# Kernel optimization log

Hardware: AMD Instinct MI355X
Metric: run time of the kernel (lower is better)

## Reference

```python
import jax, jax.numpy as jnp
import numpy as np

WEIGHT_SCALE = 0.02  # matches torch.randn(...)*0.02 init

def setup_inputs() -> dict:
    key = jax.random.key(0)
    k1, k2, k3, k4 = jax.random.split(key, 4)
    B, D = 16384, 1024
    x_re = jax.random.normal(k1, (B, D), dtype=jnp.float32)
    x_im = jax.random.normal(k2, (B, D), dtype=jnp.float32)
    w_re = jax.random.normal(k3, (D, D), dtype=jnp.float32) * WEIGHT_SCALE
    w_im = jax.random.normal(k4, (D, D), dtype=jnp.float32) * WEIGHT_SCALE
    return {"x_re": x_re, "x_im": x_im, "w_re": w_re, "w_im": w_im}

def reference(x_re, x_im, w_re, w_im):
    x = jax.lax.complex(x_re, x_im)            # [B, D] complex64
    W = jax.lax.complex(w_re, w_im)            # [D, D] complex64
    # Skew-Hermitian part: A = W - W^H
    A = W - jnp.conj(W.T)
    D = W.shape[0]
    I = jnp.eye(D, dtype=W.dtype)
    # Cayley transform: U = (I - A)^{-1} (I + A)  (unitary)
    U = jnp.linalg.solve(I - A, I + A)
    # Original: x @ U.transpose(-1, -2) (plain transpose, no conj)
    return x @ U.T
```

## Files before the change

### kernel.cpp

```cpp
#include <hip/hip_runtime.h>
#include <hip/hip_bf16.h>

#define DD 1024
#define NB 16384
#define SZ (DD * DD)
#define CHB 512

typedef unsigned short u16;
typedef __attribute__((ext_vector_type(4))) float f32x4;
typedef __attribute__((ext_vector_type(8))) short short8;
typedef __attribute__((ext_vector_type(4))) short short4v;

__device__ __forceinline__ u16 f32_bf16(float f) {
  unsigned u = __builtin_bit_cast(unsigned, f);
  u += 0x7FFFu + ((u >> 16) & 1u);
  return (u16)(u >> 16);
}
__device__ __forceinline__ float bf16_f32(u16 h) {
  unsigned u = ((unsigned)h) << 16;
  return __builtin_bit_cast(float, u);
}
__device__ __forceinline__ void gload16(const void* g, void* l) {
  __builtin_amdgcn_global_load_lds(
      (const __attribute__((address_space(1))) unsigned int*)g,
      (__attribute__((address_space(3))) unsigned int*)l, 16, 0, 0);
}

struct CArgs {
  const u16 *Ar[3], *Ai[3];
  const u16 *Br[3], *Bi[3];
  int nseg;
  float alpha, g1, g2, ddiag;
  const u16 *e1r, *e1i, *e2r, *e2i;
  u16 *hi_n_re, *hi_n_im, *lo_n_re, *lo_n_im;
  u16 *t1_re, *t1_im;
  u16 *t2_re, *t2_im;
  u16 *lt_re, *lt_im;
  int t_ldt;
  unsigned t1_xi;
  const float *cxr, *cxi; u16 *cxb;
  int cm0a, cm1a, cm0b, cm1b;
};

__global__ __launch_bounds__(256) void zchain(CArgs g) {
  constexpr int SA = 64 * 32, SB = 32 * 32;
  constexpr int SLOT = 2 * SA + 2 * SB;
  __shared__ __align__(16) u16 smem[4 * SLOT];
  const int tid = threadIdx.x;

  if ((int)blockIdx.x >= CHB) {
    int nra = g.cm1a - g.cm0a;
    int tot = nra + (g.cm1b - g.cm0b);
    for (int r = (int)blockIdx.x - CHB; r < tot; r += 256) {
      int m = (r < nra) ? (g.cm0a + r) : (g.cm0b + r - nra);
      f32x4 v = ((const f32x4*)g.cxr)[m * 256 + tid];
      short4v s;
      #pragma unroll
      for (int e = 0; e < 4; ++e) s[e] = (short)f32_bf16(v[e]);
      ((short4v*)g.cxb)[m * 512 + tid] = s;
      f32x4 w = ((const f32x4*)g.cxi)[m * 256 + tid];
      #pragma unroll
      for (int e = 0; e < 4; ++e) s[e] = (short)f32_bf16(w[e]);
      ((short4v*)g.cxb)[m * 512 + 256 + tid] = s;
    }
    return;
  }

  const int lane = tid & 63, wave = tid >> 6;
  const int wr = wave >> 1, wc = wave & 1;
  const int l15 = lane & 15, lg = lane >> 4;

  const int lin = blockIdx.x;
  const int xcd = lin & 7, tt = lin >> 3;
  const int by = (xcd >> 2) * 8 + (tt >> 3);
  const int bx = (xcd & 3) * 8 + (tt & 7);
  const int m0 = by * 64, n0 = bx * 32;

  const int arow = tid >> 2, agc = tid & 3;
  const int offA = (m0 + arow) * DD + ((agc ^ ((arow >> 1) & 3)) * 8);
  const int ldsA = tid * 8;
  const int bplane = tid >> 7, bcc = tid & 127;
  const int brow = bcc >> 2, bgc = bcc & 3;
  const int offB = (n0 + brow) * DD + ((bgc ^ ((brow >> 1) & 3)) * 8);
  const int ldsB = 2 * SA + bplane * SB + bcc * 8;

  const int slotR = lg ^ ((l15 >> 1) & 3);
  int frA[2];
  #pragma unroll
  for (int mf = 0; mf < 2; ++mf)
    frA[mf] = (wr * 32 + mf * 16 + l15) * 32 + slotR * 8;
  const int frB = (wc * 16 + l15) * 32 + slotR * 8;

  const int nt = g.nseg * 32;

  auto ISSUE = [&](int b) {
    if (b >= nt) return;
    int s = b >> 5, kk = (b & 31) << 5;
    u16* base = smem + (b & 3) * SLOT;
    gload16(g.Ar[s] + offA + kk, base + ldsA);
    gload16(g.Ai[s] + offA + kk, base + SA + ldsA);
    const u16* bptr = bplane ? g.Bi[s] : g.Br[s];
    gload16(bptr + offB + kk, base + ldsB);
  };

  f32x4 accre[2] = {};
  f32x4 accim[2] = {};

  ISSUE(0); ISSUE(1); ISSUE(2);
  asm volatile("s_waitcnt vmcnt(6)" ::: "memory");
  __builtin_amdgcn_s_barrier();

  for (int b = 0; b < nt; ++b) {
    ISSUE(b + 3);
    const u16* base = smem + (b & 3) * SLOT;
    short8 ar[2], ai[2];
    #pragma unroll
    for (int mf = 0; mf < 2; ++mf) {
      ar[mf] = *(const short8*)(base + frA[mf]);
      ai[mf] = *(const short8*)(base + SA + frA[mf]);
    }
    short8 br = *(const short8*)(base + 2 * SA + frB);
    short8 bi = *(const short8*)(base + 2 * SA + SB + frB);
    short8 bin;
    #pragma unroll
    for (int e = 0; e < 8; ++e) bin[e] = (short)(bi[e] ^ (short)0x8000);
    __builtin_amdgcn_s_setprio(1);
    #pragma unroll
    for (int mf = 0; mf < 2; ++mf) {
      accre[mf] = __builtin_amdgcn_mfma_f32_16x16x32_bf16(ar[mf], br,  accre[mf], 0, 0, 0);
      accre[mf] = __builtin_amdgcn_mfma_f32_16x16x32_bf16(ai[mf], bin, accre[mf], 0, 0, 0);
      accim[mf] = __builtin_amdgcn_mfma_f32_16x16x32_bf16(ar[mf], bi,  accim[mf], 0, 0, 0);
      accim[mf] = __builtin_amdgcn_mfma_f32_16x16x32_bf16(ai[mf], br,  accim[mf], 0, 0, 0);
    }
    __builtin_amdgcn_s_setprio(0);
    int rem = nt - 1 - b;
    if (rem >= 3)      asm volatile("s_waitcnt vmcnt(6)" ::: "memory");
    else if (rem == 2) asm volatile("s_waitcnt vmcnt(3)" ::: "memory");
    else if (rem == 1) asm volatile("s_waitcnt vmcnt(0)" ::: "memory");
    if (rem) __builtin_amdgcn_s_barrier();
  }

  u16 hre[2][4], hie[2][4], lre[2][4], lie[2][4];
  #pragma unroll
  for (int mf = 0; mf < 2; ++mf)
  #pragma unroll
  for (int r = 0; r < 4; ++r) {
    int gr = m0 + wr * 32 + mf * 16 + lg * 4 + r;
    int gc = n0 + wc * 16 + l15;
    size_t idx = (size_t)gr * DD + gc;
    float v = g.alpha * accre[mf][r];
    float w = g.alpha * accim[mf][r];
    if (g.e1r) { v += g.g1 * bf16_f32(g.e1r[idx]); w += g.g1 * bf16_f32(g.e1i[idx]); }
    if (g.e2r) { v += g.g2 * bf16_f32(g.e2r[idx]); w += g.g2 * bf16_f32(g.e2i[idx]); }
    if (gr == gc) v += g.ddiag;
    u16 h1 = f32_bf16(v); hre[mf][r] = h1;
    u16 h2 = f32_bf16(w); hie[mf][r] = h2;
    lre[mf][r] = f32_bf16(v - bf16_f32(h1));
    lie[mf][r] = f32_bf16(w - bf16_f32(h2));
    if (g.hi_n_re) { g.hi_n_re[idx] = h1; g.hi_n_im[idx] = h2; }
    if (g.lo_n_re) { g.lo_n_re[idx] = lre[mf][r]; g.lo_n_im[idx] = lie[mf][r]; }
  }

  auto bounce = [&](u16 (&vals)[2][4], u16* outp, unsigned xorm) {
    if (!outp) return;
    __syncthreads();
    #pragma unroll
    for (int mf = 0; mf < 2; ++mf)
    #pragma unroll
    for (int r = 0; r < 4; ++r) {
      int row = wr * 32 + mf * 16 + lg * 4 + r;
      int col = wc * 16 + l15;
      smem[row * 34 + col] = vals[mf][r];
    }
    __syncthreads();
    if (tid < 128) {
      int col = tid & 31, mb = (tid >> 5) * 16;
      short8 s0, s1;
      #pragma unroll
      for (int j = 0; j < 8; ++j) s0[j] = (short)(smem[(mb + j) * 34 + col] ^ xorm);
      #pragma unroll
      for (int j = 0; j < 8; ++j) s1[j] = (short)(smem[(mb + 8 + j) * 34 + col] ^ xorm);
      u16* p = outp + (size_t)(n0 + col) * g.t_ldt + m0 + mb;
      *(short8*)p = s0; *(short8*)(p + 8) = s1;
    }
  };

  bounce(hre, g.t1_re, 0);
  bounce(hie, g.t1_im, g.t1_xi);
  bounce(hre, g.t2_re, 0);
  bounce(hie, g.t2_im, 0);
  bounce(lre, g.lt_re, 0);
  bounce(lie, g.lt_im, 0);
}

#define RG_SLOT2 (2 * 256 * 64)
#define RG_LDS_BYTES (2 * RG_SLOT2 * 2)
#define RG_TILES 32

__global__ __launch_bounds__(512, 2) void rgemm(
    const u16* __restrict__ A, const u16* __restrict__ B,
    float* __restrict__ out, int ostride, int ooff)
{
  extern __shared__ u16 smem[];
  const int tid = threadIdx.x, lane = tid & 63, wave = tid >> 6;
  const int wr = wave >> 2, wc = wave & 3;
  const int l15 = lane & 15, lg = lane >> 4;

  int bx, by;
  { int lin = blockIdx.y * gridDim.x + blockIdx.x;
    int orig = (lin & 7) * 32 + (lin >> 3);
    bx = orig & 3; by = orig >> 2; }
  const int m0 = by * 256, n0 = bx * 256;

  const u16* __restrict__ Abase = A + (size_t)m0 * 2048;
  const u16* __restrict__ Bbase = B + (size_t)n0 * 2048;

  int gofsA[2], gofsB[2], lofs[2];
  #pragma unroll
  for (int i = 0; i < 2; ++i) {
    int c = i * 512 + tid;
    int sub = c >> 3;
    int sl = (c & 7) ^ (sub & 7);
    int rowA = (sub & 63) + 128 * (sub >> 6);
    int rowB = (sub & 31) + 64 * (sub >> 5);
    gofsA[i] = rowA * 2048 + sl * 8;
    gofsB[i] = rowB * 2048 + sl * 8;
    lofs[i] = c * 8;
  }

  int raf[8], rbf[8];
  #pragma unroll
  for (int mf = 0; mf < 4; ++mf)
    #pragma unroll
    for (int k = 0; k < 2; ++k)
      raf[mf * 2 + k] = (wr * 64 + mf * 16 + l15) * 64 +
                        (((k * 4 + lg) ^ (l15 & 7)) * 8);
  #pragma unroll
  for (int nf = 0; nf < 2; ++nf)
    #pragma unroll
    for (int k = 0; k < 2; ++k)
      rbf[nf * 2 + k] = (wc * 32 + nf * 16 + l15) * 64 +
                        (((k * 4 + lg) ^ (l15 & 7)) * 8);

  f32x4 acc[8][4] = {};
  short8 aA[8], bb[8];

#define MFMA_Q(mb, nb)                                                        \
  _Pragma("unroll")                                                           \
  for (int mf = 0; mf < 4; ++mf)                                              \
    _Pragma("unroll")                                                         \
    for (int nf = 0; nf < 2; ++nf)                                            \
      _Pragma("unroll")                                                       \
      for (int k = 0; k < 2; ++k)                                             \
        acc[(mb) + mf][(nb) + nf] = __builtin_amdgcn_mfma_f32_16x16x32_bf16(  \
            aA[mf * 2 + k], bb[((nb) + nf) * 2 + k], acc[(mb) + mf][(nb) + nf], 0, 0, 0);

  {
    gload16(Abase + gofsA[0], smem + lofs[0]);
    gload16(Abase + gofsA[1], smem + lofs[1]);
    gload16(Bbase + gofsB[0], smem + 16384 + lofs[0]);
    gload16(Bbase + gofsB[1], smem + 16384 + lofs[1]);
    gload16(Bbase + gofsB[0] + 32 * 2048, smem + 16384 + 8192 + lofs[0]);
    gload16(Bbase + gofsB[1] + 32 * 2048, smem + 16384 + 8192 + lofs[1]);
    gload16(Abase + gofsA[0] + 64 * 2048, smem + 8192 + lofs[0]);
    gload16(Abase + gofsA[1] + 64 * 2048, smem + 8192 + lofs[1]);
    gload16(Abase + gofsA[0] + 64, smem + RG_SLOT2 + lofs[0]);
    gload16(Abase + gofsA[1] + 64, smem + RG_SLOT2 + lofs[1]);
    gload16(Bbase + gofsB[0] + 64, smem + RG_SLOT2 + 16384 + lofs[0]);
    gload16(Bbase + gofsB[1] + 64, smem + RG_SLOT2 + 16384 + lofs[1]);
  }
  asm volatile("s_waitcnt vmcnt(4)" ::: "memory");
  __builtin_amdgcn_s_barrier();

  auto TILE = [&](int t, int gate, bool st01, bool st23) {
    const int b = t & 1;
    const u16* bA = smem + b * RG_SLOT2;
    const u16* bB = bA + 16384;
    u16* sOpp  = smem + (b ^ 1) * RG_SLOT2;
    u16* sSame = smem + b * RG_SLOT2;
    #pragma unroll
    for (int i = 0; i < 8; ++i) aA[i] = *(const short8*)(bA + raf[i]);
    #pragma unroll
    for (int i = 0; i < 4; ++i) bb[i] = *(const short8*)(bB + rbf[i]);
    if (st01) {
      int kk = (t + 1) * 64;
      gload16(Bbase + gofsB[0] + 32 * 2048 + kk, sOpp + 16384 + 8192 + lofs[0]);
      gload16(Bbase + gofsB[1] + 32 * 2048 + kk, sOpp + 16384 + 8192 + lofs[1]);
    }
    asm volatile("s_waitcnt lgkmcnt(8)" ::: "memory");
    __builtin_amdgcn_s_barrier();
    asm volatile("s_waitcnt lgkmcnt(0)" ::: "memory");
    __builtin_amdgcn_sched_barrier(0);
    __builtin_amdgcn_s_setprio(1);
    MFMA_Q(0, 0);
    __builtin_amdgcn_s_setprio(0);
    __builtin_amdgcn_s_barrier();
    #pragma unroll
    for (int i = 0; i < 4; ++i) bb[4 + i] = *(const short8*)(bB + 8192 + rbf[i]);
    if (st01) {
      int kk = (t + 1) * 64;
      gload16(Abase + gofsA[0] + 64 * 2048 + kk, sOpp + 8192 + lofs[0]);
      gload16(Abase + gofsA[1] + 64 * 2048 + kk, sOpp + 8192 + lofs[1]);
    }
    __builtin_amdgcn_s_barrier();
    asm volatile("s_waitcnt lgkmcnt(0)" ::: "memory");
    __builtin_amdgcn_sched_barrier(0);
    __builtin_amdgcn_s_setprio(1);
    MFMA_Q(0, 2);
    __builtin_amdgcn_s_setprio(0);
    __builtin_amdgcn_s_barrier();
    #pragma unroll
    for (int i = 0; i < 8; ++i) aA[i] = *(const short8*)(bA + 8192 + raf[i]);
    if (st23) {
      int kk = (t + 2) * 64;
      gload16(Abase + gofsA[0] + kk, sSame + lofs[0]);
      gload16(Abase + gofsA[1] + kk, sSame + lofs[1]);
    }
    __builtin_amdgcn_s_barrier();
    asm volatile("s_waitcnt lgkmcnt(0)" ::: "memory");
    __builtin_amdgcn_sched_barrier(0);
    __builtin_amdgcn_s_setprio(1);
    MFMA_Q(4, 0);
    __builtin_amdgcn_s_setprio(0);
    __builtin_amdgcn_s_barrier();
    if (st23) {
      int kk = (t + 2) * 64;
      gload16(Bbase + gofsB[0] + kk, sSame + 16384 + lofs[0]);
      gload16(Bbase + gofsB[1] + kk, sSame + 16384 + lofs[1]);
    }
    __builtin_amdgcn_s_barrier();
    __builtin_amdgcn_sched_barrier(0);
    __builtin_amdgcn_s_setprio(1);
    MFMA_Q(4, 2);
    __builtin_amdgcn_s_setprio(0);
    if (gate == 4)      asm volatile("s_waitcnt vmcnt(4)" ::: "memory");
    else if (gate == 0) asm volatile("s_waitcnt vmcnt(0)" ::: "memory");
    if (gate >= 0) __builtin_amdgcn_s_barrier();
  };

  for (int t = 0; t < RG_TILES - 2; ++t) TILE(t, 4, true, true);
  TILE(RG_TILES - 2, 0, true, false);
  TILE(RG_TILES - 1, -1, false, false);
#undef MFMA_Q

  #pragma unroll
  for (int mf = 0; mf < 8; ++mf)
  #pragma unroll
  for (int nf = 0; nf < 4; ++nf)
  #pragma unroll
  for (int r = 0; r < 4; ++r) {
    int gr = m0 + wr * 128 + mf * 16 + lg * 4 + r;
    int gc = n0 + wc * 64 + nf * 16 + l15;
    out[((size_t)gr * DD + gc) * ostride + ooff] = acc[mf][nf][r];
  }
}

__global__ __launch_bounds__(256) void prep_w(
    const float* __restrict__ wre, const float* __restrict__ wim,
    u16* Shr, u16* Shi_, u16* Slr, u16* Sli, u16* Snr)
{
  __shared__ float tr[32][33], ti[32][33];
  const int tx = threadIdx.x, ty = threadIdx.y;
  const int bx = blockIdx.x, by = blockIdx.y;
  #pragma unroll
  for (int k = 0; k < 4; ++k) {
    int r = bx * 32 + ty + 8 * k, c = by * 32 + tx;
    tr[ty + 8 * k][tx] = wre[r * DD + c];
    ti[ty + 8 * k][tx] = wim[r * DD + c];
  }
  __syncthreads();
  #pragma unroll
  for (int k = 0; k < 4; ++k) {
    int i = by * 32 + ty + 8 * k, j = bx * 32 + tx;
    float wr_ij = wre[i * DD + j], wi_ij = wim[i * DD + j];
    float wr_ji = tr[tx][ty + 8 * k], wi_ji = ti[tx][ty + 8 * k];
    float Sre = wr_ji - wr_ij;
    float Sim = wi_ij + wi_ji;
    int idx = i * DD + j;
    u16 h1 = f32_bf16(Sre); Shr[idx] = h1; Slr[idx] = f32_bf16(Sre - bf16_f32(h1));
    u16 h2 = f32_bf16(Sim); Shi_[idx] = h2; Sli[idx] = f32_bf16(Sim - bf16_f32(h2));
    Snr[idx] = (u16)(h1 ^ 0x8000u);
  }
}

__global__ __launch_bounds__(256) void prep_x2(
    const float* __restrict__ xr, const float* __restrict__ xi,
    u16* __restrict__ xb, int m0a, int m1a, int m0b, int m1b)
{
  int nra = m1a - m0a;
  int tot = nra + (m1b - m0b);
  const int tid = threadIdx.x;
  for (int r = blockIdx.x; r < tot; r += gridDim.x) {
    int m = (r < nra) ? (m0a + r) : (m0b + r - nra);
    f32x4 v = ((const f32x4*)xr)[m * 256 + tid];
    short4v s;
    #pragma unroll
    for (int e = 0; e < 4; ++e) s[e] = (short)f32_bf16(v[e]);
    ((short4v*)xb)[m * 512 + tid] = s;
    f32x4 w = ((const f32x4*)xi)[m * 256 + tid];
    #pragma unroll
    for (int e = 0; e < 4; ++e) s[e] = (short)f32_bf16(w[e]);
    ((short4v*)xb)[m * 512 + 256 + tid] = s;
  }
}

extern "C" void kernel_launch(void* const* d_in, const int* in_sizes, int n_in,
                              void* d_out, int out_size, void* d_ws, size_t ws_size,
                              hipStream_t stream)
{
  const float* xr  = (const float*)d_in[0];
  const float* xi  = (const float*)d_in[1];
  const float* wre = (const float*)d_in[2];
  const float* wim = (const float*)d_in[3];
  const bool realOut = (out_size == NB * DD);

  u16* P0 = (u16*)d_ws;
  auto PL = [&](int k) { return P0 + (size_t)k * SZ; };
  u16 *Shr = PL(0), *Shi_ = PL(1), *Slr = PL(2), *Sli = PL(3), *Snr = PL(4);
  u16 *Cn_r = PL(5), *Cn_i = PL(6), *Ct_r = PL(7), *Ct_i = PL(8);
  u16 *Rn_r = PL(9), *Rn_i = PL(10);
  u16 *XA_hn_r = PL(11), *XA_hn_i = PL(12), *XA_ht_r = PL(13), *XA_ht_i = PL(14);
  u16 *XB_hn_r = PL(19), *XB_hn_i = PL(20), *XB_ht_r = PL(21), *XB_ht_i = PL(22);
  u16 *XB_ln_r = PL(23), *XB_ln_i = PL(24), *XB_lt_r = PL(25), *XB_lt_i = PL(26);
  u16 *T_ht_r = PL(29), *T_ht_i = PL(30), *T_lt_r = PL(31), *T_lt_i = PL(32);
  u16 *pack1 = PL(33);
  u16 *pack2 = PL(35);
  u16 *xb    = PL(0);

  dim3 blk(256);
  prep_w<<<dim3(32, 32), dim3(32, 8), 0, stream>>>(
      wre, wim, Shr, Shi_, Slr, Sli, Snr);

  auto chain = [&](CArgs& a, int p0, int p1, int p0b, int p1b) {
    a.cxr = xr; a.cxi = xi; a.cxb = xb;
    a.cm0a = p0 * 512; a.cm1a = p1 * 512;
    a.cm0b = p0b * 512; a.cm1b = p1b * 512;
    zchain<<<dim3(CHB + 256), blk, 0, stream>>>(a);
  };
  auto base = [&]() { CArgs a{}; a.nseg = 1; a.t_ldt = DD; return a; };

  { CArgs a = base();
    a.Ar[0] = Shr; a.Ai[0] = Shi_; a.Br[0] = Snr; a.Bi[0] = Shi_;
    a.alpha = 1.f;
    a.hi_n_re = Cn_r; a.hi_n_im = Cn_i; a.t1_re = Ct_r; a.t1_im = Ct_i;
    chain(a, 15, 19, 0, 0); }
  { CArgs a = base();
    a.Ar[0] = Cn_r; a.Ai[0] = Cn_i; a.Br[0] = Ct_r; a.Bi[0] = Ct_i;
    a.alpha = 0.0212604f; a.g1 = 0.2381155f; a.e1r = Cn_r; a.e1i = Cn_i;
    a.ddiag = 0.7910964f;
    a.hi_n_re = Rn_r; a.hi_n_im = Rn_i;
    chain(a, 27, 29, 0, 0); }
  { CArgs a = base();
    a.Ar[0] = Rn_r; a.Ai[0] = Rn_i; a.Br[0] = Snr; a.Bi[0] = Shi_;
    a.alpha = 1.f; a.g1 = 1.f; a.e1r = Rn_r; a.e1i = Rn_i;
    a.hi_n_re = XA_hn_r; a.hi_n_im = XA_hn_i; a.t1_re = XA_ht_r; a.t1_im = XA_ht_i;
    chain(a, 0, 0, 0, 0); }
  { CArgs a = base();
    a.Ar[0] = Shr; a.Ai[0] = Shi_; a.Br[0] = XA_ht_r; a.Bi[0] = XA_ht_i;
    a.alpha = -1.f; a.g1 = 1.f; a.e1r = XA_hn_r; a.e1i = XA_hn_i;
    a.t1_re = T_ht_r; a.t1_im = T_ht_i;
    chain(a, 4, 8, 0, 0); }
  { CArgs a = base();
    a.Ar[0] = XA_hn_r; a.Ai[0] = XA_hn_i; a.Br[0] = T_ht_r; a.Bi[0] = T_ht_i;
    a.alpha = -1.f; a.g1 = 2.f; a.e1r = XA_hn_r; a.e1i = XA_hn_i;
    a.hi_n_re = XB_hn_r; a.hi_n_im = XB_hn_i; a.t1_re = XB_ht_r; a.t1_im = XB_ht_i;
    a.lo_n_re = XB_ln_r; a.lo_n_im = XB_ln_i; a.lt_re = XB_lt_r; a.lt_im = XB_lt_i;
    chain(a, 8, 11, 0, 0); }
  { CArgs a = base();
    a.nseg = 3;
    a.Ar[0] = Shr; a.Ai[0] = Shi_; a.Br[0] = XB_ht_r; a.Bi[0] = XB_ht_i;
    a.Ar[1] = Shr; a.Ai[1] = Shi_; a.Br[1] = XB_lt_r; a.Bi[1] = XB_lt_i;
    a.Ar[2] = Slr; a.Ai[2] = Sli;  a.Br[2] = XB_ht_r; a.Bi[2] = XB_ht_i;
    a.alpha = -1.f;
    a.g1 = 1.f; a.e1r = XB_hn_r; a.e1i = XB_hn_i;
    a.g2 = 1.f; a.e2r = XB_ln_r; a.e2i = XB_ln_i;
    a.t1_re = T_ht_r; a.t1_im = T_ht_i; a.lt_re = T_lt_r; a.lt_im = T_lt_i;
    chain(a, 11, 15, 0, 0); }
  { CArgs a = base();
    a.nseg = 2;
    a.Ar[0] = XB_hn_r; a.Ai[0] = XB_hn_i; a.Br[0] = T_ht_r; a.Bi[0] = T_ht_i;
    a.Ar[1] = XB_hn_r; a.Ai[1] = XB_hn_i; a.Br[1] = T_lt_r; a.Bi[1] = T_lt_i;
    a.alpha = -2.f;
    a.g1 = 4.f; a.e1r = XB_hn_r; a.e1i = XB_hn_i;
    a.g2 = 2.f; a.e2r = XB_ln_r; a.e2i = XB_ln_i;
    a.ddiag = -1.f;
    a.t_ldt = 2048;
    a.t1_re = pack1; a.t1_im = pack1 + 1024; a.t1_xi = 0x8000u;
    if (!realOut) { a.t2_im = pack2; a.t2_re = pack2 + 1024; }
    chain(a, 0, 4, 0, 0); }

  prep_x2<<<dim3(1024), blk, 0, stream>>>(
      xr, xi, xb, 19 * 512, 27 * 512, 29 * 512, 32 * 512);

  (void)hipFuncSetAttribute((const void*)rgemm,
      hipFuncAttributeMaxDynamicSharedMemorySize, RG_LDS_BYTES);
  dim3 gB(DD / 256, NB / 256);
  if (realOut) {
    rgemm<<<gB, dim3(512), RG_LDS_BYTES, stream>>>(xb, pack1, (float*)d_out, 1, 0);
  } else {
    rgemm<<<gB, dim3(512), RG_LDS_BYTES, stream>>>(xb, pack1, (float*)d_out, 2, 0);
    rgemm<<<gB, dim3(512), RG_LDS_BYTES, stream>>>(xb, pack2, (float*)d_out, 2, 1);
  }
}
```

Before: 323.1 us.

## Enlarge zchain tiles to 64x64 with 512 threads and two-stage K pipeline

The complex chain GEMM kernel now uses 512-thread blocks with 64x64 output tiles instead of 256 threads with 64x32, halving the block count. Loads are split evenly between the A and B planes, and the K loop processes two stages per barrier with a simpler vmcnt(0) wait. This reduces redundant A-tile reloads and barrier count, at the cost of fewer blocks to fill the CUs and a shallower prefetch lookahead. The conversion blocks and the transpose bounce are also adapted to 512 threads.

Measured after the change: 313.4 us. 1.03x faster.

```diff
diff --git a/kernel.cpp b/kernel.cpp
--- a/kernel.cpp
+++ b/kernel.cpp
@@ -4,9 +4,10 @@
 #define DD 1024
 #define NB 16384
 #define SZ (DD * DD)
-#define CHB 512
+#define CHB 256
 
 typedef unsigned short u16;
+typedef __attribute__((ext_vector_type(2))) float f32x2;
 typedef __attribute__((ext_vector_type(4))) float f32x4;
 typedef __attribute__((ext_vector_type(8))) short short8;
 typedef __attribute__((ext_vector_type(4))) short short4v;
@@ -42,8 +43,8 @@
   int cm0a, cm1a, cm0b, cm1b;
 };
 
-__global__ __launch_bounds__(256) void zchain(CArgs g) {
-  constexpr int SA = 64 * 32, SB = 32 * 32;
+__global__ __launch_bounds__(512, 2) void zchain(CArgs g) {
+  constexpr int SA = 64 * 32, SB = 64 * 32;
   constexpr int SLOT = 2 * SA + 2 * SB;
   __shared__ __align__(16) u16 smem[4 * SLOT];
   const int tid = threadIdx.x;
@@ -51,38 +52,34 @@
   if ((int)blockIdx.x >= CHB) {
     int nra = g.cm1a - g.cm0a;
     int tot = nra + (g.cm1b - g.cm0b);
+    const int chalf = tid >> 8, ct = tid & 255;
+    const float* csrc = chalf ? g.cxi : g.cxr;
     for (int r = (int)blockIdx.x - CHB; r < tot; r += 256) {
       int m = (r < nra) ? (g.cm0a + r) : (g.cm0b + r - nra);
-      f32x4 v = ((const f32x4*)g.cxr)[m * 256 + tid];
+      f32x4 v = ((const f32x4*)csrc)[m * 256 + ct];
       short4v s;
       #pragma unroll
       for (int e = 0; e < 4; ++e) s[e] = (short)f32_bf16(v[e]);
-      ((short4v*)g.cxb)[m * 512 + tid] = s;
-      f32x4 w = ((const f32x4*)g.cxi)[m * 256 + tid];
-      #pragma unroll
-      for (int e = 0; e < 4; ++e) s[e] = (short)f32_bf16(w[e]);
-      ((short4v*)g.cxb)[m * 512 + 256 + tid] = s;
+      ((short4v*)g.cxb)[m * 512 + chalf * 256 + ct] = s;
     }
     return;
   }
 
   const int lane = tid & 63, wave = tid >> 6;
-  const int wr = wave >> 1, wc = wave & 1;
+  const int wr = wave >> 2;
+  const int wc = wave & 3;
   const int l15 = lane & 15, lg = lane >> 4;
 
   const int lin = blockIdx.x;
   const int xcd = lin & 7, tt = lin >> 3;
-  const int by = (xcd >> 2) * 8 + (tt >> 3);
-  const int bx = (xcd & 3) * 8 + (tt & 7);
-  const int m0 = by * 64, n0 = bx * 32;
-
-  const int arow = tid >> 2, agc = tid & 3;
-  const int offA = (m0 + arow) * DD + ((agc ^ ((arow >> 1) & 3)) * 8);
-  const int ldsA = tid * 8;
-  const int bplane = tid >> 7, bcc = tid & 127;
-  const int brow = bcc >> 2, bgc = bcc & 3;
-  const int offB = (n0 + brow) * DD + ((bgc ^ ((brow >> 1) & 3)) * 8);
-  const int ldsB = 2 * SA + bplane * SB + bcc * 8;
+  const int by = (xcd >> 1) * 4 + (tt >> 3);
+  const int bx = (xcd & 1) * 8 + (tt & 7);
+  const int m0 = by * 64, n0 = bx * 64;
+
+  const int half = tid >> 8, w8 = tid & 255;
+  const int srow = w8 >> 2, sq = w8 & 3;
+  const int offP = ((half ? n0 : m0) + srow) * DD + ((sq ^ ((srow >> 1) & 3)) * 8);
+  const int lds0 = half * 2 * SA + w8 * 8;
 
   const int slotR = lg ^ ((l15 >> 1) & 3);
   int frA[2];
@@ -97,47 +94,50 @@
     if (b >= nt) return;
     int s = b >> 5, kk = (b & 31) << 5;
     u16* base = smem + (b & 3) * SLOT;
-    gload16(g.Ar[s] + offA + kk, base + ldsA);
-    gload16(g.Ai[s] + offA + kk, base + SA + ldsA);
-    const u16* bptr = bplane ? g.Bi[s] : g.Br[s];
-    gload16(bptr + offB + kk, base + ldsB);
+    const u16* p0 = half ? g.Br[s] : g.Ar[s];
+    const u16* p1 = half ? g.Bi[s] : g.Ai[s];
+    gload16(p0 + offP + kk, base + lds0);
+    gload16(p1 + offP + kk, base + lds0 + SA);
   };
 
   f32x4 accre[2] = {};
   f32x4 accim[2] = {};
 
-  ISSUE(0); ISSUE(1); ISSUE(2);
-  asm volatile("s_waitcnt vmcnt(6)" ::: "memory");
+  ISSUE(0); ISSUE(1);
+  asm volatile("s_waitcnt vmcnt(0)" ::: "memory");
   __builtin_amdgcn_s_barrier();
 
-  for (int b = 0; b < nt; ++b) {
-    ISSUE(b + 3);
-    const u16* base = smem + (b & 3) * SLOT;
-    short8 ar[2], ai[2];
-    #pragma unroll
-    for (int mf = 0; mf < 2; ++mf) {
-      ar[mf] = *(const short8*)(base + frA[mf]);
-      ai[mf] = *(const short8*)(base + SA + frA[mf]);
-    }
-    short8 br = *(const short8*)(base + 2 * SA + frB);
-    short8 bi = *(const short8*)(base + 2 * SA + SB + frB);
-    short8 bin;
-    #pragma unroll
-    for (int e = 0; e < 8; ++e) bin[e] = (short)(bi[e] ^ (short)0x8000);
-    __builtin_amdgcn_s_setprio(1);
-    #pragma unroll
-    for (int mf = 0; mf < 2; ++mf) {
-      accre[mf] = __builtin_amdgcn_mfma_f32_16x16x32_bf16(ar[mf], br,  accre[mf], 0, 0, 0);
-      accre[mf] = __builtin_amdgcn_mfma_f32_16x16x32_bf16(ai[mf], bin, accre[mf], 0, 0, 0);
-      accim[mf] = __builtin_amdgcn_mfma_f32_16x16x32_bf16(ar[mf], bi,  accim[mf], 0, 0, 0);
-      accim[mf] = __builtin_amdgcn_mfma_f32_16x16x32_bf16(ai[mf], br,  accim[mf], 0, 0, 0);
-    }
-    __builtin_amdgcn_s_setprio(0);
-    int rem = nt - 1 - b;
-    if (rem >= 3)      asm volatile("s_waitcnt vmcnt(6)" ::: "memory");
-    else if (rem == 2) asm volatile("s_waitcnt vmcnt(3)" ::: "memory");
-    else if (rem == 1) asm volatile("s_waitcnt vmcnt(0)" ::: "memory");
-    if (rem) __builtin_amdgcn_s_barrier();
+  for (int b = 0; b < nt; b += 2) {
+    ISSUE(b + 2); ISSUE(b + 3);
+
+    #pragma unroll
+    for (int h2 = 0; h2 < 2; ++h2) {
+      const u16* base = smem + ((b + h2) & 3) * SLOT;
+      short8 ar[2], ai[2], br, bi, bin;
+      #pragma unroll
+      for (int mf = 0; mf < 2; ++mf) {
+        ar[mf] = *(const short8*)(base + frA[mf]);
+        ai[mf] = *(const short8*)(base + SA + frA[mf]);
+      }
+      br = *(const short8*)(base + 2 * SA + frB);
+      bi = *(const short8*)(base + 2 * SA + SB + frB);
+      #pragma unroll
+      for (int e = 0; e < 8; ++e) bin[e] = (short)(bi[e] ^ (short)0x8000);
+      __builtin_amdgcn_s_setprio(1);
+      #pragma unroll
+      for (int mf = 0; mf < 2; ++mf) {
+        accre[mf] = __builtin_amdgcn_mfma_f32_16x16x32_bf16(ar[mf], br,  accre[mf], 0, 0, 0);
+        accre[mf] = __builtin_amdgcn_mfma_f32_16x16x32_bf16(ai[mf], bin, accre[mf], 0, 0, 0);
+        accim[mf] = __builtin_amdgcn_mfma_f32_16x16x32_bf16(ar[mf], bi,  accim[mf], 0, 0, 0);
+        accim[mf] = __builtin_amdgcn_mfma_f32_16x16x32_bf16(ai[mf], br,  accim[mf], 0, 0, 0);
+      }
+      __builtin_amdgcn_s_setprio(0);
+    }
+
+    if (b + 2 < nt) {
+      asm volatile("s_waitcnt vmcnt(0)" ::: "memory");
+      __builtin_amdgcn_s_barrier();
+    }
   }
 
   u16 hre[2][4], hie[2][4], lre[2][4], lie[2][4];
@@ -170,18 +170,16 @@
     for (int r = 0; r < 4; ++r) {
       int row = wr * 32 + mf * 16 + lg * 4 + r;
       int col = wc * 16 + l15;
-      smem[row * 34 + col] = vals[mf][r];
+      smem[row * 66 + col] = vals[mf][r];
     }
     __syncthreads();
-    if (tid < 128) {
-      int col = tid & 31, mb = (tid >> 5) * 16;
-      short8 s0, s1;
+    {
+      int col = tid & 63, mb = (tid >> 6) * 8;
+      short8 s0;
       #pragma unroll
-      for (int j = 0; j < 8; ++j) s0[j] = (short)(smem[(mb + j) * 34 + col] ^ xorm);
-      #pragma unroll
-      for (int j = 0; j < 8; ++j) s1[j] = (short)(smem[(mb + 8 + j) * 34 + col] ^ xorm);
+      for (int j = 0; j < 8; ++j) s0[j] = (short)(smem[(mb + j) * 66 + col] ^ xorm);
       u16* p = outp + (size_t)(n0 + col) * g.t_ldt + m0 + mb;
-      *(short8*)p = s0; *(short8*)(p + 8) = s1;
+      *(short8*)p = s0;
     }
   };
 
@@ -435,7 +433,7 @@
     a.cxr = xr; a.cxi = xi; a.cxb = xb;
     a.cm0a = p0 * 512; a.cm1a = p1 * 512;
     a.cm0b = p0b * 512; a.cm1b = p1b * 512;
-    zchain<<<dim3(CHB + 256), blk, 0, stream>>>(a);
+    zchain<<<dim3(CHB + 256), dim3(512), 0, stream>>>(a);
   };
   auto base = [&]() { CArgs a{}; a.nseg = 1; a.t_ldt = DD; return a; };
 
```
